# Kernel optimization log

Measured on AMD Instinct MI355X. Metric: run time of the kernel, lower is better.

The kernel has to match this reference:

```python
import jax, jax.numpy as jnp
import numpy as np


def conv2d_reflect(x, w, b, stride):
    # 3x3 conv, padding=1, padding_mode='reflect'
    x = jnp.pad(x, ((0, 0), (0, 0), (1, 1), (1, 1)), mode='reflect')
    y = jax.lax.conv_general_dilated(x, w, (stride, stride), 'VALID',
                                     dimension_numbers=('NCHW', 'OIHW', 'NCHW'))
    return y + b[None, :, None, None]


def avg_pool(x, k):
    B, C, H, W = x.shape
    return x.reshape(B, C, H // k, k, W // k, k).mean(axis=(3, 5))


def _interp_axis(x, size_out, axis):
    # 1D linear interpolation with align_corners=True semantics
    size_in = x.shape[axis]
    pos = jnp.linspace(0.0, size_in - 1.0, size_out)
    i0 = jnp.clip(jnp.floor(pos).astype(jnp.int32), 0, size_in - 2)
    frac = (pos - i0.astype(x.dtype))
    shape = [1] * x.ndim
    shape[axis] = size_out
    frac = frac.reshape(shape)
    a = jnp.take(x, i0, axis=axis)
    b = jnp.take(x, i0 + 1, axis=axis)
    return a + frac * (b - a)


def resize_bilinear_ac(x, oh, ow):
    return _interp_axis(_interp_axis(x, oh, 2), ow, 3)


def _forward(img, conv1_w, conv1_b, conv2_w, conv2_b, conv3_w, conv3_b,
             conv4_w, conv4_b, lin1_w, lin1_b, lin2_w, lin2_b, luts):
    B, C, H, W = img.shape
    silu = jax.nn.silu
    # --- feature branch on fixed 256x256 resize ---
    x = resize_bilinear_ac(img, 256, 256)
    c1 = silu(conv2d_reflect(x, conv1_w, conv1_b, 2))    # [B,32,128,128]
    c2 = silu(conv2d_reflect(c1, conv2_w, conv2_b, 2))   # [B,64,64,64]
    c3 = silu(conv2d_reflect(c2, conv3_w, conv3_b, 2))   # [B,128,32,32]
    c4 = silu(conv2d_reflect(c3, conv4_w, conv4_b, 2))   # [B,256,16,16]
    feat = jnp.concatenate([avg_pool(c1, 16), avg_pool(c2, 8),
                            avg_pool(c3, 4), avg_pool(c4, 2)], axis=1)  # [B,480,8,8]
    h1 = silu(conv2d_reflect(feat, lin1_w, lin1_b, 1))   # [B,128,8,8]
    wl = jax.lax.conv_general_dilated(h1, lin2_w, (1, 1), 'VALID',
                                      dimension_numbers=('NCHW', 'OIHW', 'NCHW'))
    wl = jax.nn.sigmoid(wl + lin2_b[None, :, None, None])  # [B,27,8,8]
    weights = resize_bilinear_ac(wl, H, W)               # [B, C*K, H, W]
    # --- adaptive 1D LUT transform (per-pixel interpolated gather) ---
    Cl, K, N = luts.shape
    pos = jnp.clip(img, 0.0, 1.0) * (N - 1)
    i0 = jnp.clip(jnp.floor(pos).astype(jnp.int32), 0, N - 2)  # [B,C,H,W]
    frac = pos - i0.astype(pos.dtype)
    cidx = jnp.arange(Cl)[None, :, None, None, None]
    kidx = jnp.arange(K)[None, None, :, None, None]
    iexp = i0[:, :, None, :, :]
    v0 = luts[cidx, kidx, iexp]          # [B,C,K,H,W]
    v1 = luts[cidx, kidx, iexp + 1]
    val = v0 + frac[:, :, None, :, :] * (v1 - v0)
    wts = weights.reshape(B, Cl, K, H, W)
    return jnp.einsum('bckhw,bckhw->bchw', wts, val)


def setup_inputs() -> dict:
    key = jax.random.key(0)
    ks = jax.random.split(key, 10)
    s = 0.05
    return {
        'img': jax.random.uniform(ks[0], (2, 3, 1024, 1024), dtype=jnp.float32),
        'conv1_w': jax.random.normal(ks[1], (32, 3, 3, 3), dtype=jnp.float32) * s,
        'conv1_b': jnp.zeros((32,), jnp.float32),
        'conv2_w': jax.random.normal(ks[2], (64, 32, 3, 3), dtype=jnp.float32) * s,
        'conv2_b': jnp.zeros((64,), jnp.float32),
        'conv3_w': jax.random.normal(ks[3], (128, 64, 3, 3), dtype=jnp.float32) * s,
        'conv3_b': jnp.zeros((128,), jnp.float32),
        'conv4_w': jax.random.normal(ks[4], (256, 128, 3, 3), dtype=jnp.float32) * s,
        'conv4_b': jnp.zeros((256,), jnp.float32),
        'lin1_w': jax.random.normal(ks[5], (128, 480, 3, 3), dtype=jnp.float32) * s,
        'lin1_b': jnp.zeros((128,), jnp.float32),
        'lin2_w': jax.random.normal(ks[6], (27, 128, 1, 1), dtype=jnp.float32) * s,
        'lin2_b': jnp.zeros((27,), jnp.float32),
        'luts': jax.random.normal(ks[7], (3, 9, 256), dtype=jnp.float32),
    }


def reference(img, conv1_w, conv1_b, conv2_w, conv2_b, conv3_w, conv3_b,
              conv4_w, conv4_b, lin1_w, lin1_b, lin2_w, lin2_b, luts):
    out = _forward(img, conv1_w, conv1_b, conv2_w, conv2_b, conv3_w, conv3_b,
                   conv4_w, conv4_b, lin1_w, lin1_b, lin2_w, lin2_b, luts)
    return jnp.clip(out, 0.0, 1.0)
```

## Files before the change

kernel.cpp:

```cpp
#include <hip/hip_runtime.h>

#define DI __device__ __forceinline__

DI float silu_f(float x) { return x / (1.f + __expf(-x)); }
DI float sigmoid_f(float x) { return 1.f / (1.f + __expf(-x)); }
DI int reflect_i(int i, int n) { if (i < 0) i = -i; if (i >= n) i = 2 * n - 2 - i; return i; }

__global__ __launch_bounds__(256) void k_resize(const float* __restrict__ img,
                                                float* __restrict__ x) {
    __shared__ float r0s[1024], r1s[1024];
    const int oy = blockIdx.x & 255;
    const int bc = blockIdx.x >> 8;
    float py = oy * (1023.f / 255.f);
    int iy0 = (int)py; if (iy0 > 1022) iy0 = 1022;
    float fy = py - (float)iy0;
    const float* p0 = img + ((size_t)bc * 1024 + iy0) * 1024;
    ((float4*)r0s)[threadIdx.x] = ((const float4*)p0)[threadIdx.x];
    ((float4*)r1s)[threadIdx.x] = ((const float4*)(p0 + 1024))[threadIdx.x];
    __syncthreads();
    const int ox = threadIdx.x;
    float px = ox * (1023.f / 255.f);
    int ix0 = (int)px; if (ix0 > 1022) ix0 = 1022;
    float fx = px - (float)ix0;
    float a00 = r0s[ix0], a01 = r0s[ix0 + 1];
    float a10 = r1s[ix0], a11 = r1s[ix0 + 1];
    float r0v = a00 + fy * (a10 - a00);
    float r1v = a01 + fy * (a11 - a01);
    x[((size_t)bc * 256 + oy) * 256 + ox] = r0v + fx * (r1v - r0v);
}

template<int CIN, int HIN, int WIN, int COUT, int OCW>
__global__ __launch_bounds__(256) void k_conv_woc(const float* __restrict__ in,
                                                  const float* __restrict__ w,
                                                  const float* __restrict__ bias,
                                                  float* __restrict__ out) {
    constexpr int HOUT = HIN / 2, WOUT = WIN / 2;
    constexpr int NB_PX = 2 * HOUT * WOUT / 64;
    constexpr int NOC = 4 * OCW;

    __shared__ float sw[NOC * CIN * 12];
    const int tid = threadIdx.x;
    const int ocu = blockIdx.x / NB_PX;
    const int bpx = blockIdx.x % NB_PX;
    {
        const float* src = w + (size_t)(ocu * NOC) * CIN * 9;
        for (int i = tid; i < NOC * CIN * 9; i += 256)
            sw[(i / 9) * 12 + (i % 9)] = src[i];
    }
    __syncthreads();

    const int wave = tid >> 6, lane = tid & 63;
    const int pxu = bpx * 64 + lane;
    const int ox = pxu % WOUT;
    const int oy = (pxu / WOUT) % HOUT;
    const int bb = pxu / (WOUT * HOUT);

    int iy[3], xs[3];
#pragma unroll
    for (int k = 0; k < 3; ++k) {
        iy[k] = reflect_i(2 * oy + k - 1, HIN);
        xs[k] = reflect_i(2 * ox + k - 1, WIN);
    }

    float acc[OCW];
#pragma unroll
    for (int o = 0; o < OCW; ++o) acc[o] = 0.f;

    for (int ic = 0; ic < CIN; ++ic) {
        const float* ib = in + ((size_t)bb * CIN + ic) * HIN * WIN;
        float t[3][3];
#pragma unroll
        for (int ky = 0; ky < 3; ++ky) {
            const float* rp = ib + iy[ky] * WIN;
#pragma unroll
            for (int kx = 0; kx < 3; ++kx) t[ky][kx] = rp[xs[kx]];
        }
#pragma unroll
        for (int o = 0; o < OCW; ++o) {
            const float* wp = sw + ((size_t)(wave * OCW + o) * CIN + ic) * 12;
            float wv[9];
#pragma unroll
            for (int j = 0; j < 9; ++j) wv[j] = wp[j];
#pragma unroll
            for (int ky = 0; ky < 3; ++ky)
#pragma unroll
                for (int kx = 0; kx < 3; ++kx)
                    acc[o] = fmaf(t[ky][kx], wv[ky * 3 + kx], acc[o]);
        }
    }

#pragma unroll
    for (int o = 0; o < OCW; ++o) {
        const int oc = ocu * NOC + wave * OCW + o;
        out[(((size_t)bb * COUT + oc) * HOUT + oy) * WOUT + ox] =
            silu_f(acc[o] + bias[oc]);
    }
}

template<int CIN, int HIN, int WIN, int COUT, int OC_PER>
__global__ __launch_bounds__(256) void k_conv_w4(const float* __restrict__ in,
                                                 const float* __restrict__ w,
                                                 const float* __restrict__ bias,
                                                 float* __restrict__ out) {
    constexpr int HOUT = HIN / 2, WOUT = WIN / 2;
    constexpr int NB_PX = 2 * HOUT * WOUT / 64;
    constexpr int ICC = CIN / 4;

    __shared__ float sw[OC_PER * CIN * 12];
    __shared__ float sred[4][OC_PER][64];
    const int tid = threadIdx.x;
    const int ocu = blockIdx.x / NB_PX;
    const int bpx = blockIdx.x % NB_PX;
    {
        const float* src = w + (size_t)(ocu * OC_PER) * CIN * 9;
        for (int i = tid; i < OC_PER * CIN * 9; i += 256)
            sw[(i / 9) * 12 + (i % 9)] = src[i];
    }
    __syncthreads();

    const int kc = tid >> 6;
    const int lane = tid & 63;
    const int pxu = bpx * 64 + lane;
    const int ox = pxu % WOUT;
    const int oy = (pxu / WOUT) % HOUT;
    const int bb = pxu / (WOUT * HOUT);

    int iy[3], xs[3];
#pragma unroll
    for (int k = 0; k < 3; ++k) {
        iy[k] = reflect_i(2 * oy + k - 1, HIN);
        xs[k] = reflect_i(2 * ox + k - 1, WIN);
    }

    float acc[OC_PER];
#pragma unroll
    for (int o = 0; o < OC_PER; ++o) acc[o] = 0.f;

    for (int icl = 0; icl < ICC; ++icl) {
        const int ic = kc * ICC + icl;
        const float* ib = in + ((size_t)bb * CIN + ic) * HIN * WIN;
        float t[3][3];
#pragma unroll
        for (int ky = 0; ky < 3; ++ky) {
            const float* rp = ib + iy[ky] * WIN;
#pragma unroll
            for (int kx = 0; kx < 3; ++kx) t[ky][kx] = rp[xs[kx]];
        }
#pragma unroll
        for (int o = 0; o < OC_PER; ++o) {
            const float* wp = sw + ((size_t)o * CIN + ic) * 12;
            float wv[9];
#pragma unroll
            for (int j = 0; j < 9; ++j) wv[j] = wp[j];
#pragma unroll
            for (int ky = 0; ky < 3; ++ky)
#pragma unroll
                for (int kx = 0; kx < 3; ++kx)
                    acc[o] = fmaf(t[ky][kx], wv[ky * 3 + kx], acc[o]);
        }
    }

#pragma unroll
    for (int o = 0; o < OC_PER; ++o) sred[kc][o][lane] = acc[o];
    __syncthreads();
    if (kc < OC_PER) {
        const int o = kc;
        const int oc = ocu * OC_PER + o;
        float s = sred[0][o][lane] + sred[1][o][lane] + sred[2][o][lane] + sred[3][o][lane];
        out[(((size_t)bb * COUT + oc) * HOUT + oy) * WOUT + ox] = silu_f(s + bias[oc]);
    }
}

__global__ __launch_bounds__(256) void k_pool(const float* __restrict__ c1,
                                              const float* __restrict__ c2,
                                              const float* __restrict__ c3,
                                              const float* __restrict__ c4,
                                              float* __restrict__ feat) {
    const int tid = threadIdx.x;
    const int W = blockIdx.x * 4 + (tid >> 6);
    const int lane = tid & 63;
    if (W < 512) {
        int bb = W >> 8, rem = W & 255;
        int c = rem >> 3, y = rem & 7;
        const float* p = c1 + ((size_t)bb * 32 + c) * 128 * 128 + (y * 16) * 128 + lane * 2;
        float s = 0.f;
#pragma unroll
        for (int r = 0; r < 16; ++r) {
            float2 v = *(const float2*)(p + r * 128);
            s += v.x + v.y;
        }
        s += __shfl_xor(s, 1, 64);
        s += __shfl_xor(s, 2, 64);
        s += __shfl_xor(s, 4, 64);
        if ((lane & 7) == 0)
            feat[((size_t)bb * 480 + c) * 64 + y * 8 + (lane >> 3)] = s * (1.f / 256.f);
    } else if (W < 1536) {
        int V = W - 512;
        int bb = V >> 9, rem = V & 511;
        int c = rem >> 3, y = rem & 7;
        const float* p = c2 + ((size_t)bb * 64 + c) * 64 * 64 + (y * 8) * 64 + lane;
        float s = 0.f;
#pragma unroll
        for (int r = 0; r < 8; ++r) s += p[r * 64];
        s += __shfl_xor(s, 1, 64);
        s += __shfl_xor(s, 2, 64);
        s += __shfl_xor(s, 4, 64);
        if ((lane & 7) == 0)
            feat[((size_t)bb * 480 + 32 + c) * 64 + y * 8 + (lane >> 3)] = s * (1.f / 64.f);
    } else if (W < 1792) {
        int T = (W - 1536) * 64 + lane;
        int bb = T >> 13, rem = T & 8191;
        int c = rem >> 6, y = (rem >> 3) & 7, x = rem & 7;
        const float* p = c3 + ((size_t)bb * 128 + c) * 32 * 32 + (y * 4) * 32 + x * 4;
        float s = 0.f;
#pragma unroll
        for (int r = 0; r < 4; ++r) {
            float4 v = *(const float4*)(p + r * 32);
            s += v.x + v.y + v.z + v.w;
        }
        feat[((size_t)bb * 480 + 96 + c) * 64 + y * 8 + x] = s * (1.f / 16.f);
    } else {
        int T = (W - 1792) * 64 + lane;
        int bb = T >> 14, rem = T & 16383;
        int c = rem >> 6, y = (rem >> 3) & 7, x = rem & 7;
        const float* p = c4 + ((size_t)bb * 256 + c) * 16 * 16 + (y * 2) * 16 + x * 2;
        float2 v0 = *(const float2*)p;
        float2 v1 = *(const float2*)(p + 16);
        feat[((size_t)bb * 480 + 224 + c) * 64 + y * 8 + x] = (v0.x + v0.y + v1.x + v1.y) * 0.25f;
    }
}

__global__ __launch_bounds__(512) void k_lin1(const float* __restrict__ feat,
                                              const float* __restrict__ w,
                                              const float* __restrict__ bias,
                                              float* __restrict__ h1) {
    __shared__ float sw[480 * 9];
    __shared__ float sred[8][64];
    const int tid = threadIdx.x;
    const int bb = blockIdx.x >> 7;
    const int oc = blockIdx.x & 127;
    {
        const float* src = w + (size_t)oc * 480 * 9;
        for (int i = tid; i < 480 * 9; i += 512) sw[i] = src[i];
    }
    const int wave = tid >> 6;
    const int lane = tid & 63;
    const int py = lane >> 3, px = lane & 7;
    int srcl[9];
#pragma unroll
    for (int ky = 0; ky < 3; ++ky)
#pragma unroll
        for (int kx = 0; kx < 3; ++kx)
            srcl[ky * 3 + kx] = reflect_i(py + ky - 1, 8) * 8 + reflect_i(px + kx - 1, 8);
    __syncthreads();

    const float* fp = feat + (size_t)bb * 480 * 64;
    float acc = 0.f;
    for (int ic = wave * 60; ic < wave * 60 + 60; ++ic) {
        float v = fp[ic * 64 + lane];
        const float* wp = sw + ic * 9;
#pragma unroll
        for (int j = 0; j < 9; ++j)
            acc = fmaf(__shfl(v, srcl[j], 64), wp[j], acc);
    }
    sred[wave][lane] = acc;
    __syncthreads();
    if (wave == 0) {
        float s = 0.f;
#pragma unroll
        for (int wv = 0; wv < 8; ++wv) s += sred[wv][lane];
        h1[((size_t)bb * 128 + oc) * 64 + lane] = silu_f(s + bias[oc]);
    }
}

__global__ void k_lin2(const float* __restrict__ h1, const float* __restrict__ w,
                       const float* __restrict__ bias, float* __restrict__ wl) {
    int idx = blockIdx.x * blockDim.x + threadIdx.x;
    if (idx >= 2 * 27 * 64) return;
    int pix = idx & 63;
    int oc = (idx >> 6) % 27;
    int bb = idx / (27 * 64);
    const float* hp = h1 + (size_t)bb * 128 * 64 + pix;
    const float* wp = w + oc * 128;
    float sum = bias[oc];
    for (int ic = 0; ic < 128; ++ic) sum = fmaf(hp[ic * 64], wp[ic], sum);
    wl[((size_t)bb * 27 + oc) * 64 + pix] = sigmoid_f(sum);
}

__global__ __launch_bounds__(256) void k_apply(const float* __restrict__ img,
                                               const float* __restrict__ wl,
                                               const float* __restrict__ luts,
                                               float* __restrict__ out) {
    __shared__ float2 slut2[9 * 256];
    __shared__ float swl[9 * 64];
    __shared__ float su4[4 * 72];
    const int tid = threadIdx.x;
    const int bc = blockIdx.y;
    const int bb = bc / 3, c = bc % 3;

    for (int i = tid; i < 9 * 256; i += 256) {
        int k = i >> 8, j = i & 255;
        const float* lp = luts + (size_t)(c * 9 + k) * 256;
        float v0 = lp[j];
        float v1 = lp[j < 255 ? j + 1 : 255];
        slut2[i] = make_float2(v0, v1);
    }
    for (int i = tid; i < 9 * 64; i += 256)
        swl[i] = wl[((size_t)bb * 27 + c * 9) * 64 + i];
    __syncthreads();
    for (int i = tid; i < 288; i += 256) {
        int rr = i / 72, rem = i % 72;
        int k = rem >> 3, xx = rem & 7;
        int h = blockIdx.x * 4 + rr;
        float py = h * (7.f / 1023.f);
        int iy0 = (int)py; if (iy0 > 6) iy0 = 6;
        float fy = py - (float)iy0;
        float a = swl[k * 64 + iy0 * 8 + xx];
        float b = swl[k * 64 + iy0 * 8 + 8 + xx];
        su4[i] = fmaf(fy, b - a, a);
    }
    __syncthreads();

    const int x0 = tid * 4;
    float fx[4]; int sel[4]; int cbase;
    {
        float p0 = x0 * (7.f / 1023.f);
        int ib = (int)p0; if (ib > 6) ib = 6;
        cbase = ib;
#pragma unroll
        for (int p = 0; p < 4; ++p) {
            float pxf = (x0 + p) * (7.f / 1023.f);
            int i = (int)pxf; if (i > 6) i = 6;
            sel[p] = i - cbase;
            fx[p] = pxf - (float)i;
        }
    }
    const size_t plane = ((size_t)bb * 3 + c) * 1024;
    const int h0 = blockIdx.x * 4;

    float4 v = ((const float4*)(img + (plane + h0) * 1024))[tid];
    for (int rr = 0; rr < 4; ++rr) {
        float4 vn = v;
        if (rr < 3) vn = ((const float4*)(img + (plane + h0 + rr + 1) * 1024))[tid];
        float xin[4] = {v.x, v.y, v.z, v.w};
        int i0[4]; float fr[4]; float acc[4] = {0.f, 0.f, 0.f, 0.f};
#pragma unroll
        for (int p = 0; p < 4; ++p) {
            float pv = fminf(fmaxf(xin[p], 0.f), 1.f) * 255.f;
            int i = (int)pv; if (i > 254) i = 254;
            i0[p] = i; fr[p] = pv - (float)i;
        }
        const float* srow = su4 + rr * 72;
#pragma unroll
        for (int k = 0; k < 9; ++k) {
            float s0 = srow[k * 8 + cbase];
            float s1 = srow[k * 8 + cbase + 1];
            float s2 = (cbase < 6) ? srow[k * 8 + cbase + 2] : s1;
            const float2* lrow = slut2 + k * 256;
#pragma unroll
            for (int p = 0; p < 4; ++p) {
                float a = sel[p] ? s1 : s0;
                float b = sel[p] ? s2 : s1;
                float wt = fmaf(fx[p], b - a, a);
                float2 l = lrow[i0[p]];
                acc[p] = fmaf(wt, fmaf(fr[p], l.y - l.x, l.x), acc[p]);
            }
        }
        float4 o4 = make_float4(fminf(fmaxf(acc[0], 0.f), 1.f),
                                fminf(fmaxf(acc[1], 0.f), 1.f),
                                fminf(fmaxf(acc[2], 0.f), 1.f),
                                fminf(fmaxf(acc[3], 0.f), 1.f));
        ((float4*)(out + (plane + h0 + rr) * 1024))[tid] = o4;
        v = vn;
    }
}

extern "C" void kernel_launch(void* const* d_in, const int* in_sizes, int n_in,
                              void* d_out, int out_size, void* d_ws, size_t ws_size,
                              hipStream_t stream) {
    const float* img     = (const float*)d_in[0];
    const float* conv1_w = (const float*)d_in[1];
    const float* conv1_b = (const float*)d_in[2];
    const float* conv2_w = (const float*)d_in[3];
    const float* conv2_b = (const float*)d_in[4];
    const float* conv3_w = (const float*)d_in[5];
    const float* conv3_b = (const float*)d_in[6];
    const float* conv4_w = (const float*)d_in[7];
    const float* conv4_b = (const float*)d_in[8];
    const float* lin1_w  = (const float*)d_in[9];
    const float* lin1_b  = (const float*)d_in[10];
    const float* lin2_w  = (const float*)d_in[11];
    const float* lin2_b  = (const float*)d_in[12];
    const float* luts    = (const float*)d_in[13];
    float* out = (float*)d_out;

    float* ws = (float*)d_ws;
    float* x_rs = ws;            ws += 2 * 3 * 256 * 256;
    float* c1   = ws;            ws += 2 * 32 * 128 * 128;
    float* c2   = ws;            ws += 2 * 64 * 64 * 64;
    float* c3   = ws;            ws += 2 * 128 * 32 * 32;
    float* c4   = ws;            ws += 2 * 256 * 16 * 16;
    float* feat = ws;            ws += 2 * 480 * 8 * 8;
    float* h1   = ws;            ws += 2 * 128 * 8 * 8;
    float* wl   = ws;            ws += 2 * 27 * 8 * 8;

    const int B = 256;
    k_resize<<<6 * 256, B, 0, stream>>>(img, x_rs);
    k_conv_woc<3, 256, 256, 32, 2><<<2048, B, 0, stream>>>(x_rs, conv1_w, conv1_b, c1);
    k_conv_woc<32, 128, 128, 64, 1><<<2048, B, 0, stream>>>(c1, conv2_w, conv2_b, c2);
    k_conv_w4<64, 64, 64, 128, 2><<<2048, B, 0, stream>>>(c2, conv3_w, conv3_b, c3);
    k_conv_w4<128, 32, 32, 256, 1><<<2048, B, 0, stream>>>(c3, conv4_w, conv4_b, c4);
    k_pool<<<576, B, 0, stream>>>(c1, c2, c3, c4, feat);
    k_lin1<<<256, 512, 0, stream>>>(feat, lin1_w, lin1_b, h1);
    k_lin2<<<(2 * 27 * 64 + B - 1) / B, B, 0, stream>>>(h1, lin2_w, lin2_b, wl);
    dim3 agrid(256, 6);
    k_apply<<<agrid, B, 0, stream>>>(img, wl, luts, out);
}
```

Before: 271.9 us.

## Unroll conv input channels, widen conv4 outputs, fuse lin2 into apply

The conv kernels now precompute the nine reflected tap offsets once per thread. The channel loop is unrolled two at a time so twice as many independent global loads are in flight before the FMAs. Conv4 now computes two output channels per block, which halves its grid and reuses each input tap across both. The separate lin2 kernel is removed: every apply block recomputes its nine sigmoid weight maps from h1, trading a launch and a round trip to global memory for redundant per-block 128-wide dot products.

New measurement: 278.5 us. 1.02x slower.

```diff
diff --git a/kernel.cpp b/kernel.cpp
--- a/kernel.cpp
+++ b/kernel.cpp
@@ -37,6 +37,7 @@
     constexpr int HOUT = HIN / 2, WOUT = WIN / 2;
     constexpr int NB_PX = 2 * HOUT * WOUT / 64;
     constexpr int NOC = 4 * OCW;
+    constexpr int PL = HIN * WIN;
 
     __shared__ float sw[NOC * CIN * 12];
     const int tid = threadIdx.x;
@@ -55,37 +56,51 @@
     const int oy = (pxu / WOUT) % HOUT;
     const int bb = pxu / (WOUT * HOUT);
 
-    int iy[3], xs[3];
-#pragma unroll
-    for (int k = 0; k < 3; ++k) {
-        iy[k] = reflect_i(2 * oy + k - 1, HIN);
-        xs[k] = reflect_i(2 * ox + k - 1, WIN);
+    int off[9];
+#pragma unroll
+    for (int ky = 0; ky < 3; ++ky) {
+        int ry = reflect_i(2 * oy + ky - 1, HIN) * WIN;
+#pragma unroll
+        for (int kx = 0; kx < 3; ++kx)
+            off[ky * 3 + kx] = ry + reflect_i(2 * ox + kx - 1, WIN);
     }
 
     float acc[OCW];
 #pragma unroll
     for (int o = 0; o < OCW; ++o) acc[o] = 0.f;
-
-    for (int ic = 0; ic < CIN; ++ic) {
-        const float* ib = in + ((size_t)bb * CIN + ic) * HIN * WIN;
-        float t[3][3];
-#pragma unroll
-        for (int ky = 0; ky < 3; ++ky) {
-            const float* rp = ib + iy[ky] * WIN;
-#pragma unroll
-            for (int kx = 0; kx < 3; ++kx) t[ky][kx] = rp[xs[kx]];
-        }
-#pragma unroll
-        for (int o = 0; o < OCW; ++o) {
-            const float* wp = sw + ((size_t)(wave * OCW + o) * CIN + ic) * 12;
-            float wv[9];
-#pragma unroll
-            for (int j = 0; j < 9; ++j) wv[j] = wp[j];
-#pragma unroll
-            for (int ky = 0; ky < 3; ++ky)
-#pragma unroll
-                for (int kx = 0; kx < 3; ++kx)
-                    acc[o] = fmaf(t[ky][kx], wv[ky * 3 + kx], acc[o]);
+    const float* swb = sw + (size_t)(wave * OCW) * CIN * 12;
+    const float* base = in + (size_t)bb * CIN * PL;
+
+    if constexpr (CIN % 2 == 0) {
+        for (int ic = 0; ic < CIN; ic += 2) {
+            float t0[9], t1[9];
+#pragma unroll
+            for (int j = 0; j < 9; ++j) t0[j] = base[off[j]];
+#pragma unroll
+            for (int j = 0; j < 9; ++j) t1[j] = base[PL + off[j]];
+#pragma unroll
+            for (int o = 0; o < OCW; ++o) {
+                const float* wp = swb + ((size_t)o * CIN + ic) * 12;
+#pragma unroll
+                for (int j = 0; j < 9; ++j) acc[o] = fmaf(t0[j], wp[j], acc[o]);
+#pragma unroll
+                for (int j = 0; j < 9; ++j) acc[o] = fmaf(t1[j], wp[12 + j], acc[o]);
+            }
+            base += 2 * PL;
+        }
+    } else {
+#pragma unroll
+        for (int ic = 0; ic < CIN; ++ic) {
+            float t0[9];
+#pragma unroll
+            for (int j = 0; j < 9; ++j) t0[j] = base[off[j]];
+#pragma unroll
+            for (int o = 0; o < OCW; ++o) {
+                const float* wp = swb + ((size_t)o * CIN + ic) * 12;
+#pragma unroll
+                for (int j = 0; j < 9; ++j) acc[o] = fmaf(t0[j], wp[j], acc[o]);
+            }
+            base += PL;
         }
     }
 
@@ -105,6 +120,8 @@
     constexpr int HOUT = HIN / 2, WOUT = WIN / 2;
     constexpr int NB_PX = 2 * HOUT * WOUT / 64;
     constexpr int ICC = CIN / 4;
+    constexpr int PL = HIN * WIN;
+    static_assert(ICC % 2 == 0, "ICC even");
 
     __shared__ float sw[OC_PER * CIN * 12];
     __shared__ float sred[4][OC_PER][64];
@@ -125,39 +142,35 @@
     const int oy = (pxu / WOUT) % HOUT;
     const int bb = pxu / (WOUT * HOUT);
 
-    int iy[3], xs[3];
-#pragma unroll
-    for (int k = 0; k < 3; ++k) {
-        iy[k] = reflect_i(2 * oy + k - 1, HIN);
-        xs[k] = reflect_i(2 * ox + k - 1, WIN);
+    int off[9];
+#pragma unroll
+    for (int ky = 0; ky < 3; ++ky) {
+        int ry = reflect_i(2 * oy + ky - 1, HIN) * WIN;
+#pragma unroll
+        for (int kx = 0; kx < 3; ++kx)
+            off[ky * 3 + kx] = ry + reflect_i(2 * ox + kx - 1, WIN);
     }
 
     float acc[OC_PER];
 #pragma unroll
     for (int o = 0; o < OC_PER; ++o) acc[o] = 0.f;
-
-    for (int icl = 0; icl < ICC; ++icl) {
-        const int ic = kc * ICC + icl;
-        const float* ib = in + ((size_t)bb * CIN + ic) * HIN * WIN;
-        float t[3][3];
-#pragma unroll
-        for (int ky = 0; ky < 3; ++ky) {
-            const float* rp = ib + iy[ky] * WIN;
-#pragma unroll
-            for (int kx = 0; kx < 3; ++kx) t[ky][kx] = rp[xs[kx]];
-        }
+    const float* base = in + ((size_t)bb * CIN + kc * ICC) * PL;
+
+    for (int icl = 0; icl < ICC; icl += 2) {
+        float t0[9], t1[9];
+#pragma unroll
+        for (int j = 0; j < 9; ++j) t0[j] = base[off[j]];
+#pragma unroll
+        for (int j = 0; j < 9; ++j) t1[j] = base[PL + off[j]];
 #pragma unroll
         for (int o = 0; o < OC_PER; ++o) {
-            const float* wp = sw + ((size_t)o * CIN + ic) * 12;
-            float wv[9];
-#pragma unroll
-            for (int j = 0; j < 9; ++j) wv[j] = wp[j];
-#pragma unroll
-            for (int ky = 0; ky < 3; ++ky)
-#pragma unroll
-                for (int kx = 0; kx < 3; ++kx)
-                    acc[o] = fmaf(t[ky][kx], wv[ky * 3 + kx], acc[o]);
-        }
+            const float* wp = sw + ((size_t)o * CIN + kc * ICC + icl) * 12;
+#pragma unroll
+            for (int j = 0; j < 9; ++j) acc[o] = fmaf(t0[j], wp[j], acc[o]);
+#pragma unroll
+            for (int j = 0; j < 9; ++j) acc[o] = fmaf(t1[j], wp[12 + j], acc[o]);
+        }
+        base += 2 * PL;
     }
 
 #pragma unroll
@@ -273,22 +286,10 @@
     }
 }
 
-__global__ void k_lin2(const float* __restrict__ h1, const float* __restrict__ w,
-                       const float* __restrict__ bias, float* __restrict__ wl) {
-    int idx = blockIdx.x * blockDim.x + threadIdx.x;
-    if (idx >= 2 * 27 * 64) return;
-    int pix = idx & 63;
-    int oc = (idx >> 6) % 27;
-    int bb = idx / (27 * 64);
-    const float* hp = h1 + (size_t)bb * 128 * 64 + pix;
-    const float* wp = w + oc * 128;
-    float sum = bias[oc];
-    for (int ic = 0; ic < 128; ++ic) sum = fmaf(hp[ic * 64], wp[ic], sum);
-    wl[((size_t)bb * 27 + oc) * 64 + pix] = sigmoid_f(sum);
-}
-
 __global__ __launch_bounds__(256) void k_apply(const float* __restrict__ img,
-                                               const float* __restrict__ wl,
+                                               const float* __restrict__ h1,
+                                               const float* __restrict__ l2w,
+                                               const float* __restrict__ l2b,
                                                const float* __restrict__ luts,
                                                float* __restrict__ out) {
     __shared__ float2 slut2[9 * 256];
@@ -297,6 +298,7 @@
     const int tid = threadIdx.x;
     const int bc = blockIdx.y;
     const int bb = bc / 3, c = bc % 3;
+    const int wave = tid >> 6, pix = tid & 63;
 
     for (int i = tid; i < 9 * 256; i += 256) {
         int k = i >> 8, j = i & 255;
@@ -305,8 +307,15 @@
         float v1 = lp[j < 255 ? j + 1 : 255];
         slut2[i] = make_float2(v0, v1);
     }
-    for (int i = tid; i < 9 * 64; i += 256)
-        swl[i] = wl[((size_t)bb * 27 + c * 9) * 64 + i];
+    {
+        const float* hp = h1 + (size_t)bb * 128 * 64;
+        for (int o = wave; o < 9; o += 4) {
+            const float* wp = l2w + (size_t)(c * 9 + o) * 128;
+            float s = l2b[c * 9 + o];
+            for (int ic = 0; ic < 128; ++ic) s = fmaf(hp[ic * 64 + pix], wp[ic], s);
+            swl[o * 64 + pix] = sigmoid_f(s);
+        }
+    }
     __syncthreads();
     for (int i = tid; i < 288; i += 256) {
         int rr = i / 72, rem = i % 72;
@@ -402,17 +411,15 @@
     float* c4   = ws;            ws += 2 * 256 * 16 * 16;
     float* feat = ws;            ws += 2 * 480 * 8 * 8;
     float* h1   = ws;            ws += 2 * 128 * 8 * 8;
-    float* wl   = ws;            ws += 2 * 27 * 8 * 8;
 
     const int B = 256;
     k_resize<<<6 * 256, B, 0, stream>>>(img, x_rs);
     k_conv_woc<3, 256, 256, 32, 2><<<2048, B, 0, stream>>>(x_rs, conv1_w, conv1_b, c1);
     k_conv_woc<32, 128, 128, 64, 1><<<2048, B, 0, stream>>>(c1, conv2_w, conv2_b, c2);
     k_conv_w4<64, 64, 64, 128, 2><<<2048, B, 0, stream>>>(c2, conv3_w, conv3_b, c3);
-    k_conv_w4<128, 32, 32, 256, 1><<<2048, B, 0, stream>>>(c3, conv4_w, conv4_b, c4);
+    k_conv_w4<128, 32, 32, 256, 2><<<1024, B, 0, stream>>>(c3, conv4_w, conv4_b, c4);
     k_pool<<<576, B, 0, stream>>>(c1, c2, c3, c4, feat);
     k_lin1<<<256, 512, 0, stream>>>(feat, lin1_w, lin1_b, h1);
-    k_lin2<<<(2 * 27 * 64 + B - 1) / B, B, 0, stream>>>(h1, lin2_w, lin2_b, wl);
     dim3 agrid(256, 6);
-    k_apply<<<agrid, B, 0, stream>>>(img, wl, luts, out);
-}
+    k_apply<<<agrid, B, 0, stream>>>(img, h1, lin2_w, lin2_b, luts, out);
+}
```
